# Optimization experiments

Hardware: AMD Instinct MI355X
Metric: run time of the kernel (lower is better)

Reference implementation:

```python
import jax, jax.numpy as jnp
import numpy as np

K = 3          # kernel size
SIZE = K * K   # 9 taps
STEPS = 10     # max_step
EPS = 1e-5


def _unfold3x3(x):
    # x: [n, c, h, w] -> patches [n, c, 9, h, w], same order as F.unfold (row-major taps)
    n, c, h, w = x.shape
    xp = jnp.pad(x, ((0, 0), (0, 0), (1, 1), (1, 1)))
    return jnp.stack([xp[:, :, di:di + h, dj:dj + w]
                      for di in range(K) for dj in range(K)], axis=2)


def setup_inputs() -> dict:
    key = jax.random.key(0)
    k1, k2 = jax.random.split(key)
    n, c, h, w = 8, 64, 128, 128
    inp = jax.random.normal(k1, (n, c, h, w), dtype=jnp.float32)
    weight = jax.random.uniform(k2, (n, SIZE, h, w), dtype=jnp.float32)  # wc=1
    return {"input": inp, "weight": weight}


def reference(input, weight):
    n, c, h, w = input.shape
    wc = weight.shape[1] // SIZE  # = 1
    wt = weight.reshape(n, wc, SIZE, h, w)
    # normalize taps to sum to 1 per pixel (non-sym_norm branch)
    norm_weight = wt / (jnp.sum(wt, axis=2, keepdims=True) + EPS)  # [n,1,9,h,w]
    x = input
    for _ in range(STEPS):
        patches = _unfold3x3(x)                 # [n,c,9,h,w]
        x = jnp.sum(patches * norm_weight, axis=2)  # [n,c,h,w]
    return x
```

## Files before the change

### kernel.cpp

```cpp
#include <hip/hip_runtime.h>
#include <hip/hip_fp16.h>


#define NB    8
#define CC    64
#define HH    128
#define WW    128
#define TAPS  9
#define PLANE (HH * WW)

#define CORE   16
#define HALO5  5
#define RROWS  26
#define RSTR4  129
#define NTH    832
#define NSTEP  5
#define CGRP   16
#define CSUB   8
#define WROWS  24
#define WCELLS (WROWS * TAPS * 32)

#define PERM4(J) ((((J) & 3) << 5) | ((J) >> 2))

typedef unsigned int u32x4 __attribute__((ext_vector_type(4)));

#define MIXLO(acc, xh, wf)                                                      \
    asm("v_fma_mix_f32 %0, %1, %2, %0 op_sel:[0,0,0] op_sel_hi:[1,0,0]"         \
        : "+v"(acc) : "v"(xh), "v"(wf))
#define MIXHI(acc, xh, wf)                                                      \
    asm("v_fma_mix_f32 %0, %1, %2, %0 op_sel:[1,0,0] op_sel_hi:[1,0,0]"         \
        : "+v"(acc) : "v"(xh), "v"(wf))
#define MIX8(aL, aH, cell, wf)                                                  \
    MIXLO(aL.x, cell.x, wf); MIXHI(aL.y, cell.x, wf);                           \
    MIXLO(aL.z, cell.y, wf); MIXHI(aL.w, cell.y, wf);                           \
    MIXLO(aH.x, cell.z, wf); MIXHI(aH.y, cell.z, wf);                           \
    MIXLO(aH.z, cell.w, wf); MIXHI(aH.w, cell.w, wf)

__device__ __forceinline__ float4 cvt_lo(const uint4 v) {
    const float2 a = __half22float2(*reinterpret_cast<const __half2*>(&v.x));
    const float2 b = __half22float2(*reinterpret_cast<const __half2*>(&v.y));
    return make_float4(a.x, a.y, b.x, b.y);
}
__device__ __forceinline__ float4 cvt_hi(const uint4 v) {
    const float2 a = __half22float2(*reinterpret_cast<const __half2*>(&v.z));
    const float2 b = __half22float2(*reinterpret_cast<const __half2*>(&v.w));
    return make_float4(a.x, a.y, b.x, b.y);
}
__device__ __forceinline__ unsigned pack2(float a, float b) {
    __half2 h = __floats2half2_rn(a, b);
    return *reinterpret_cast<unsigned*>(&h);
}
__device__ __forceinline__ float2 h22f2(unsigned u) {
    return __half22float2(*reinterpret_cast<const __half2*>(&u));
}

__global__ __launch_bounds__(256) void mp_norm_kernel(const float* __restrict__ w,
                                                      uint2* __restrict__ nwh) {
    int tid = blockIdx.x * 256 + threadIdx.x;
    int wg = tid & 31;
    int h  = (tid >> 5) & 127;
    int n  = tid >> 12;
    int base = n * TAPS * PLANE + h * WW + wg * 4;
    float4 t[TAPS];
    float sx = 1e-5f, sy = 1e-5f, sz = 1e-5f, sw = 1e-5f;
#pragma unroll
    for (int k = 0; k < TAPS; ++k) {
        t[k] = *reinterpret_cast<const float4*>(w + base + k * PLANE);
        sx += t[k].x; sy += t[k].y; sz += t[k].z; sw += t[k].w;
    }
    float rx = 1.0f / sx, ry = 1.0f / sy, rz = 1.0f / sz, rw = 1.0f / sw;
#pragma unroll
    for (int k = 0; k < TAPS; ++k) {
        uint2 v;
        v.x = pack2(t[k].x * rx, t[k].y * ry);
        v.y = pack2(t[k].z * rz, t[k].w * rw);
        nwh[((n * TAPS + k) * HH + h) * 32 + wg] = v;
    }
}

#define FUSED_PROLOGUE                                                          \
    __shared__ uint4 bufA[RROWS * RSTR4];                                       \
    __shared__ uint4 bufB[RROWS * RSTR4];                                       \
    __shared__ uint2 wlds[WCELLS];                                              \
    const int bid = blockIdx.x;                                                 \
    const int n   = bid & 7;                                                    \
    const int ht  = (bid >> 3) & 7;                                             \
    const int cg  = bid >> 6;                                                   \
    const int tr0 = ht * CORE;                                                  \
    const int cb  = cg * CGRP;                                                  \
    const int t   = threadIdx.x;                                                \
    const int row = t >> 5;                                                     \
    const int s   = t & 31;                                                     \
    {                                                                           \
        const uint2* nwb = nwh + (size_t)n * TAPS * (PLANE / 4);                \
        for (int idx = t; idx < WCELLS; idx += NTH) {                           \
            const int wrow = idx / (TAPS * 32);                                 \
            const int rem  = idx - wrow * (TAPS * 32);                          \
            const int k    = rem >> 5;                                          \
            const int ss   = rem & 31;                                          \
            const int gr   = tr0 - (HALO5 - 1) + wrow;                          \
            uint2 v = make_uint2(0u, 0u);                                       \
            if (gr >= 0 && gr < HH)                                             \
                v = nwb[(k * HH + gr) * 32 + ss];                               \
            wlds[idx] = v;                                                      \
        }                                                                       \
    }                                                                           \
    const uint4 zc = make_uint4(0u, 0u, 0u, 0u);                                \
    const float4 z = make_float4(0.f, 0.f, 0.f, 0.f);

#define FUSED_STEPS                                                             \
        uint4* pin  = bufA;                                                     \
        uint4* pout = bufB;                                                     \
        for (int st = 0; st < NSTEP; ++st) {                                    \
            const int lo = st + 1;                                              \
            const int hi = 24 - st;                                             \
            if (row >= lo && row <= hi) {                                       \
                int wb = (row - 1) * (TAPS * 32) + s;                           \
                asm volatile("" : "+v"(wb));                                    \
                float4 aL0 = z, aL1 = z, aL2 = z, aL3 = z;                      \
                float4 aH0 = z, aH1 = z, aH2 = z, aH3 = z;                      \
                _Pragma("unroll")                                               \
                for (int di = 0; di < 3; ++di) {                                \
                    const uint4* rp = pin + (row - 1 + di) * RSTR4;             \
                    uint4 x[6];                                                 \
                    x[0] = (s > 0) ? rp[96 + s - 1] : zc;                       \
                    x[1] = rp[s];                                               \
                    x[2] = rp[32 + s];                                          \
                    x[3] = rp[64 + s];                                          \
                    x[4] = rp[96 + s];                                          \
                    x[5] = (s < 31) ? rp[s + 1] : zc;                           \
                    _Pragma("unroll")                                           \
                    for (int dj = 0; dj < 3; ++dj) {                            \
                        const int k = di * 3 + dj;                              \
                        const uint2 wv = wlds[wb + k * 32];                     \
                        const float2 w01 = h22f2(wv.x);                         \
                        const float2 w23 = h22f2(wv.y);                         \
                        MIX8(aL0, aH0, x[0 + dj], w01.x);                       \
                        MIX8(aL1, aH1, x[1 + dj], w01.y);                       \
                        MIX8(aL2, aH2, x[2 + dj], w23.x);                       \
                        MIX8(aL3, aH3, x[3 + dj], w23.y);                       \
                    }                                                           \
                }                                                               \
                uint4* op = pout + row * RSTR4;                                 \
                uint4 o0, o1, o2, o3;                                           \
                o0.x = pack2(aL0.x, aL0.y); o0.y = pack2(aL0.z, aL0.w);         \
                o0.z = pack2(aH0.x, aH0.y); o0.w = pack2(aH0.z, aH0.w);         \
                o1.x = pack2(aL1.x, aL1.y); o1.y = pack2(aL1.z, aL1.w);         \
                o1.z = pack2(aH1.x, aH1.y); o1.w = pack2(aH1.z, aH1.w);         \
                o2.x = pack2(aL2.x, aL2.y); o2.y = pack2(aL2.z, aL2.w);         \
                o2.z = pack2(aH2.x, aH2.y); o2.w = pack2(aH2.z, aH2.w);         \
                o3.x = pack2(aL3.x, aL3.y); o3.y = pack2(aL3.z, aL3.w);         \
                o3.z = pack2(aH3.x, aH3.y); o3.w = pack2(aH3.z, aH3.w);         \
                op[s]      = o0;                                                \
                op[32 + s] = o1;                                                \
                op[64 + s] = o2;                                                \
                op[96 + s] = o3;                                                \
            }                                                                   \
            __syncthreads();                                                    \
            uint4* tmp = pin; pin = pout; pout = tmp;                           \
        }

__global__ __launch_bounds__(NTH, 1) void mp_fused5_a(const float* __restrict__ src,
                                                      uint4* __restrict__ dst16,
                                                      const uint2* __restrict__ nwh) {
    FUSED_PROLOGUE
    for (int ch = 0; ch < CGRP; ch += CSUB) {
        const float* sp = src + ((size_t)n * CC + cb + ch) * PLANE;
        for (int idx = t; idx < RROWS * WW; idx += NTH) {
            const int r  = idx >> 7;
            const int J  = idx & 127;
            const int gr = tr0 - HALO5 + r;
            uint4 v = zc;
            if (gr >= 0 && gr < HH) {
                const int o = gr * WW + J;
                v.x = pack2(sp[o],             sp[PLANE + o]);
                v.y = pack2(sp[2 * PLANE + o], sp[3 * PLANE + o]);
                v.z = pack2(sp[4 * PLANE + o], sp[5 * PLANE + o]);
                v.w = pack2(sp[6 * PLANE + o], sp[7 * PLANE + o]);
            }
            bufA[r * RSTR4 + PERM4(J)] = v;
        }
        __syncthreads();
        FUSED_STEPS
        uint4* dp16 = dst16 + ((size_t)n * (CC / 8) + ((cb + ch) >> 3)) * PLANE;
        for (int idx = t; idx < CORE * WW; idx += NTH) {
            const int r = idx >> 7;
            const int J = idx & 127;
            dp16[(tr0 + r) * WW + J] = pin[(r + HALO5) * RSTR4 + PERM4(J)];
        }
        __syncthreads();
    }
}

__global__ __launch_bounds__(NTH, 1) void mp_fused5_b(const uint4* __restrict__ src16,
                                                      float* __restrict__ dst,
                                                      const uint2* __restrict__ nwh) {
    FUSED_PROLOGUE
#pragma unroll 1
    for (int ch = 0; ch < CGRP; ch += CSUB) {
        const volatile u32x4* sp16v =
            (const volatile u32x4*)(src16 + ((size_t)n * (CC / 8) + ((cb + ch) >> 3)) * PLANE);
        for (int idx = t; idx < RROWS * WW; idx += NTH) {
            const int r  = idx >> 7;
            const int J  = idx & 127;
            const int gr = tr0 - HALO5 + r;
            uint4 v = zc;
            if (gr >= 0 && gr < HH) {
                const u32x4 w = sp16v[gr * WW + J];
                v = make_uint4(w.x, w.y, w.z, w.w);
            }
            bufA[r * RSTR4 + PERM4(J)] = v;
        }
        __syncthreads();
        FUSED_STEPS
        float* dp = dst + ((size_t)n * CC + cb + ch) * PLANE;
        for (int idx = t; idx < CORE * WW; idx += NTH) {
            const int r = idx >> 7;
            const int J = idx & 127;
            const uint4 v = pin[(r + HALO5) * RSTR4 + PERM4(J)];
            const float4 lo = cvt_lo(v);
            const float4 hi = cvt_hi(v);
            const int o = (tr0 + r) * WW + J;
            dp[o]             = lo.x;
            dp[PLANE + o]     = lo.y;
            dp[2 * PLANE + o] = lo.z;
            dp[3 * PLANE + o] = lo.w;
            dp[4 * PLANE + o] = hi.x;
            dp[5 * PLANE + o] = hi.y;
            dp[6 * PLANE + o] = hi.z;
            dp[7 * PLANE + o] = hi.w;
        }
        __syncthreads();
    }
}

extern "C" void kernel_launch(void* const* d_in, const int* in_sizes, int n_in,
                              void* d_out, int out_size, void* d_ws, size_t ws_size,
                              hipStream_t stream) {
    const float* input  = (const float*)d_in[0];
    const float* weight = (const float*)d_in[1];
    float* out = (float*)d_out;

    uint2* nwh = (uint2*)d_ws;
    uint4* B0  = (uint4*)((char*)d_ws + (size_t)NB * TAPS * PLANE * 2);

    mp_norm_kernel<<<128, 256, 0, stream>>>(weight, nwh);
    mp_fused5_a<<<256, NTH, 0, stream>>>(input, B0, nwh);
    mp_fused5_b<<<256, NTH, 0, stream>>>(B0, out, nwh);
}
```

Measured before the change: 87.72 us.

## Split 8-channel fp16 LDS cells into two 4-channel planes processed sequentially

Replaces each uint4 shared-memory cell holding eight fp16 channels with two separate uint2 planes of four channels each. The stencil body now runs twice per step, once per plane, keeping four accumulator float4s live instead of eight. The intermediate global buffer between the two fused kernels becomes two 4-channel planes as well. The aim is to reduce register pressure and LDS access width, at the cost of loading the weights and neighbour indices twice per step and issuing more, narrower LDS and global accesses.

```diff
diff --git a/kernel.cpp b/kernel.cpp
--- a/kernel.cpp
+++ b/kernel.cpp
@@ -22,7 +22,7 @@
 
 #define PERM4(J) ((((J) & 3) << 5) | ((J) >> 2))
 
-typedef unsigned int u32x4 __attribute__((ext_vector_type(4)));
+typedef unsigned int u32x2 __attribute__((ext_vector_type(2)));
 
 #define MIXLO(acc, xh, wf)                                                      \
     asm("v_fma_mix_f32 %0, %1, %2, %0 op_sel:[0,0,0] op_sel_hi:[1,0,0]"         \
@@ -30,22 +30,10 @@
 #define MIXHI(acc, xh, wf)                                                      \
     asm("v_fma_mix_f32 %0, %1, %2, %0 op_sel:[1,0,0] op_sel_hi:[1,0,0]"         \
         : "+v"(acc) : "v"(xh), "v"(wf))
-#define MIX8(aL, aH, cell, wf)                                                  \
-    MIXLO(aL.x, cell.x, wf); MIXHI(aL.y, cell.x, wf);                           \
-    MIXLO(aL.z, cell.y, wf); MIXHI(aL.w, cell.y, wf);                           \
-    MIXLO(aH.x, cell.z, wf); MIXHI(aH.y, cell.z, wf);                           \
-    MIXLO(aH.z, cell.w, wf); MIXHI(aH.w, cell.w, wf)
-
-__device__ __forceinline__ float4 cvt_lo(const uint4 v) {
-    const float2 a = __half22float2(*reinterpret_cast<const __half2*>(&v.x));
-    const float2 b = __half22float2(*reinterpret_cast<const __half2*>(&v.y));
-    return make_float4(a.x, a.y, b.x, b.y);
-}
-__device__ __forceinline__ float4 cvt_hi(const uint4 v) {
-    const float2 a = __half22float2(*reinterpret_cast<const __half2*>(&v.z));
-    const float2 b = __half22float2(*reinterpret_cast<const __half2*>(&v.w));
-    return make_float4(a.x, a.y, b.x, b.y);
-}
+#define MIX4(a, cell, wf)                                                       \
+    MIXLO(a.x, cell.x, wf); MIXHI(a.y, cell.x, wf);                             \
+    MIXLO(a.z, cell.y, wf); MIXHI(a.w, cell.y, wf)
+
 __device__ __forceinline__ unsigned pack2(float a, float b) {
     __half2 h = __floats2half2_rn(a, b);
     return *reinterpret_cast<unsigned*>(&h);
@@ -79,9 +67,11 @@
 }
 
 #define FUSED_PROLOGUE                                                          \
-    __shared__ uint4 bufA[RROWS * RSTR4];                                       \
-    __shared__ uint4 bufB[RROWS * RSTR4];                                       \
-    __shared__ uint2 wlds[WCELLS];                                              \
+    __shared__ uint2 xA0[RROWS * RSTR4];                     \
+    __shared__ uint2 xB0[RROWS * RSTR4];                                        \
+    __shared__ uint2 xA1[RROWS * RSTR4];                                        \
+    __shared__ uint2 xB1[RROWS * RSTR4];                                        \
+    __shared__ uint2 wlds[WCELLS];             \
     const int bid = blockIdx.x;                                                 \
     const int n   = bid & 7;                                                    \
     const int ht  = (bid >> 3) & 7;                                             \
@@ -105,63 +95,58 @@
             wlds[idx] = v;                                                      \
         }                                                                       \
     }                                                                           \
-    const uint4 zc = make_uint4(0u, 0u, 0u, 0u);                                \
-    const float4 z = make_float4(0.f, 0.f, 0.f, 0.f);
+    const uint2 zc2 = make_uint2(0u, 0u);                                       \
+    const float4 z  = make_float4(0.f, 0.f, 0.f, 0.f);
+
+#define SUB_BODY(PIN, POUT)                                                     \
+            {                                                                   \
+                float4 a0 = z, a1 = z, a2 = z, a3 = z;                          \
+                _Pragma("unroll")                                               \
+                for (int di = 0; di < 3; ++di) {                                \
+                    const uint2* rp = PIN + (row - 1 + di) * RSTR4;             \
+                    uint2 x[6];                                                 \
+                    x[0] = (s > 0) ? rp[96 + s - 1] : zc2;                      \
+                    x[1] = rp[s];                                               \
+                    x[2] = rp[32 + s];                                          \
+                    x[3] = rp[64 + s];                                          \
+                    x[4] = rp[96 + s];                                          \
+                    x[5] = (s < 31) ? rp[s + 1] : zc2;                          \
+                    _Pragma("unroll")                                           \
+                    for (int dj = 0; dj < 3; ++dj) {                            \
+                        const uint2 wv = wlds[wb + (di * 3 + dj) * 32];         \
+                        const float2 w01 = h22f2(wv.x);                         \
+                        const float2 w23 = h22f2(wv.y);                         \
+                        MIX4(a0, x[0 + dj], w01.x);                             \
+                        MIX4(a1, x[1 + dj], w01.y);                             \
+                        MIX4(a2, x[2 + dj], w23.x);                             \
+                        MIX4(a3, x[3 + dj], w23.y);                             \
+                    }                                                           \
+                }                                                               \
+                uint2* op = POUT + row * RSTR4;                                 \
+                op[s]      = make_uint2(pack2(a0.x, a0.y), pack2(a0.z, a0.w));  \
+                op[32 + s] = make_uint2(pack2(a1.x, a1.y), pack2(a1.z, a1.w));  \
+                op[64 + s] = make_uint2(pack2(a2.x, a2.y), pack2(a2.z, a2.w));  \
+                op[96 + s] = make_uint2(pack2(a3.x, a3.y), pack2(a3.z, a3.w));  \
+            }
 
 #define FUSED_STEPS                                                             \
-        uint4* pin  = bufA;                                                     \
-        uint4* pout = bufB;                                                     \
+        uint2 *pin0 = xA0, *pout0 = xB0, *pin1 = xA1, *pout1 = xB1;             \
         for (int st = 0; st < NSTEP; ++st) {                                    \
             const int lo = st + 1;                                              \
             const int hi = 24 - st;                                             \
             if (row >= lo && row <= hi) {                                       \
                 int wb = (row - 1) * (TAPS * 32) + s;                           \
                 asm volatile("" : "+v"(wb));                                    \
-                float4 aL0 = z, aL1 = z, aL2 = z, aL3 = z;                      \
-                float4 aH0 = z, aH1 = z, aH2 = z, aH3 = z;                      \
-                _Pragma("unroll")                                               \
-                for (int di = 0; di < 3; ++di) {                                \
-                    const uint4* rp = pin + (row - 1 + di) * RSTR4;             \
-                    uint4 x[6];                                                 \
-                    x[0] = (s > 0) ? rp[96 + s - 1] : zc;                       \
-                    x[1] = rp[s];                                               \
-                    x[2] = rp[32 + s];                                          \
-                    x[3] = rp[64 + s];                                          \
-                    x[4] = rp[96 + s];                                          \
-                    x[5] = (s < 31) ? rp[s + 1] : zc;                           \
-                    _Pragma("unroll")                                           \
-                    for (int dj = 0; dj < 3; ++dj) {                            \
-                        const int k = di * 3 + dj;                              \
-                        const uint2 wv = wlds[wb + k * 32];                     \
-                        const float2 w01 = h22f2(wv.x);                         \
-                        const float2 w23 = h22f2(wv.y);                         \
-                        MIX8(aL0, aH0, x[0 + dj], w01.x);                       \
-                        MIX8(aL1, aH1, x[1 + dj], w01.y);                       \
-                        MIX8(aL2, aH2, x[2 + dj], w23.x);                       \
-                        MIX8(aL3, aH3, x[3 + dj], w23.y);                       \
-                    }                                                           \
-                }                                                               \
-                uint4* op = pout + row * RSTR4;                                 \
-                uint4 o0, o1, o2, o3;                                           \
-                o0.x = pack2(aL0.x, aL0.y); o0.y = pack2(aL0.z, aL0.w);         \
-                o0.z = pack2(aH0.x, aH0.y); o0.w = pack2(aH0.z, aH0.w);         \
-                o1.x = pack2(aL1.x, aL1.y); o1.y = pack2(aL1.z, aL1.w);         \
-                o1.z = pack2(aH1.x, aH1.y); o1.w = pack2(aH1.z, aH1.w);         \
-                o2.x = pack2(aL2.x, aL2.y); o2.y = pack2(aL2.z, aL2.w);         \
-                o2.z = pack2(aH2.x, aH2.y); o2.w = pack2(aH2.z, aH2.w);         \
-                o3.x = pack2(aL3.x, aL3.y); o3.y = pack2(aL3.z, aL3.w);         \
-                o3.z = pack2(aH3.x, aH3.y); o3.w = pack2(aH3.z, aH3.w);         \
-                op[s]      = o0;                                                \
-                op[32 + s] = o1;                                                \
-                op[64 + s] = o2;                                                \
-                op[96 + s] = o3;                                                \
+                SUB_BODY(pin0, pout0)                                           \
+                SUB_BODY(pin1, pout1)                                           \
             }                                                                   \
             __syncthreads();                                                    \
-            uint4* tmp = pin; pin = pout; pout = tmp;                           \
+            uint2* t0 = pin0; pin0 = pout0; pout0 = t0;                         \
+            uint2* t1 = pin1; pin1 = pout1; pout1 = t1;                         \
         }
 
 __global__ __launch_bounds__(NTH, 1) void mp_fused5_a(const float* __restrict__ src,
-                                                      uint4* __restrict__ dst16,
+                                                      uint2* __restrict__ dst16,
                                                       const uint2* __restrict__ nwh) {
     FUSED_PROLOGUE
     for (int ch = 0; ch < CGRP; ch += CSUB) {
@@ -170,46 +155,59 @@
             const int r  = idx >> 7;
             const int J  = idx & 127;
             const int gr = tr0 - HALO5 + r;
-            uint4 v = zc;
+            uint2 v0 = zc2, v1 = zc2;
             if (gr >= 0 && gr < HH) {
                 const int o = gr * WW + J;
-                v.x = pack2(sp[o],             sp[PLANE + o]);
-                v.y = pack2(sp[2 * PLANE + o], sp[3 * PLANE + o]);
-                v.z = pack2(sp[4 * PLANE + o], sp[5 * PLANE + o]);
-                v.w = pack2(sp[6 * PLANE + o], sp[7 * PLANE + o]);
+                v0.x = pack2(sp[o],             sp[PLANE + o]);
+                v0.y = pack2(sp[2 * PLANE + o], sp[3 * PLANE + o]);
+                v1.x = pack2(sp[4 * PLANE + o], sp[5 * PLANE + o]);
+                v1.y = pack2(sp[6 * PLANE + o], sp[7 * PLANE + o]);
             }
-            bufA[r * RSTR4 + PERM4(J)] = v;
+            const int c = r * RSTR4 + PERM4(J);
+            xA0[c] = v0;
+            xA1[c] = v1;
         }
         __syncthreads();
         FUSED_STEPS
-        uint4* dp16 = dst16 + ((size_t)n * (CC / 8) + ((cb + ch) >> 3)) * PLANE;
+        const int q = (cb + ch) >> 2;
+        uint2* dp0 = dst16 + ((size_t)n * (CC / 4) + q) * PLANE;
+        uint2* dp1 = dp0 + PLANE;
         for (int idx = t; idx < CORE * WW; idx += NTH) {
             const int r = idx >> 7;
             const int J = idx & 127;
-            dp16[(tr0 + r) * WW + J] = pin[(r + HALO5) * RSTR4 + PERM4(J)];
-        }
-        __syncthreads();
-    }
-}
-
-__global__ __launch_bounds__(NTH, 1) void mp_fused5_b(const uint4* __restrict__ src16,
+            const int c = (r + HALO5) * RSTR4 + PERM4(J);
+            const int o = (tr0 + r) * WW + J;
+            dp0[o] = pin0[c];
+            dp1[o] = pin1[c];
+        }
+        __syncthreads();
+    }
+}
+
+__global__ __launch_bounds__(NTH, 1) void mp_fused5_b(const uint2* __restrict__ src16,
                                                       float* __restrict__ dst,
                                                       const uint2* __restrict__ nwh) {
     FUSED_PROLOGUE
 #pragma unroll 1
     for (int ch = 0; ch < CGRP; ch += CSUB) {
-        const volatile u32x4* sp16v =
-            (const volatile u32x4*)(src16 + ((size_t)n * (CC / 8) + ((cb + ch) >> 3)) * PLANE);
+        const int q = (cb + ch) >> 2;
+        const volatile u32x2* s0 =
+            (const volatile u32x2*)(src16 + ((size_t)n * (CC / 4) + q) * PLANE);
+        const volatile u32x2* s1 = s0 + PLANE;
         for (int idx = t; idx < RROWS * WW; idx += NTH) {
             const int r  = idx >> 7;
             const int J  = idx & 127;
             const int gr = tr0 - HALO5 + r;
-            uint4 v = zc;
+            uint2 v0 = zc2, v1 = zc2;
             if (gr >= 0 && gr < HH) {
-                const u32x4 w = sp16v[gr * WW + J];
-                v = make_uint4(w.x, w.y, w.z, w.w);
+                const u32x2 w0 = s0[gr * WW + J];
+                const u32x2 w1 = s1[gr * WW + J];
+                v0 = make_uint2(w0.x, w0.y);
+                v1 = make_uint2(w1.x, w1.y);
             }
-            bufA[r * RSTR4 + PERM4(J)] = v;
+            const int c = r * RSTR4 + PERM4(J);
+            xA0[c] = v0;
+            xA1[c] = v1;
         }
         __syncthreads();
         FUSED_STEPS
@@ -217,18 +215,22 @@
         for (int idx = t; idx < CORE * WW; idx += NTH) {
             const int r = idx >> 7;
             const int J = idx & 127;
-            const uint4 v = pin[(r + HALO5) * RSTR4 + PERM4(J)];
-            const float4 lo = cvt_lo(v);
-            const float4 hi = cvt_hi(v);
+            const int c = (r + HALO5) * RSTR4 + PERM4(J);
+            const uint2 v0 = pin0[c];
+            const uint2 v1 = pin1[c];
+            const float2 c01 = h22f2(v0.x);
+            const float2 c23 = h22f2(v0.y);
+            const float2 c45 = h22f2(v1.x);
+            const float2 c67 = h22f2(v1.y);
             const int o = (tr0 + r) * WW + J;
-            dp[o]             = lo.x;
-            dp[PLANE + o]     = lo.y;
-            dp[2 * PLANE + o] = lo.z;
-            dp[3 * PLANE + o] = lo.w;
-            dp[4 * PLANE + o] = hi.x;
-            dp[5 * PLANE + o] = hi.y;
-            dp[6 * PLANE + o] = hi.z;
-            dp[7 * PLANE + o] = hi.w;
+            dp[o]             = c01.x;
+            dp[PLANE + o]     = c01.y;
+            dp[2 * PLANE + o] = c23.x;
+            dp[3 * PLANE + o] = c23.y;
+            dp[4 * PLANE + o] = c45.x;
+            dp[5 * PLANE + o] = c45.y;
+            dp[6 * PLANE + o] = c67.x;
+            dp[7 * PLANE + o] = c67.y;
         }
         __syncthreads();
     }
@@ -242,7 +244,7 @@
     float* out = (float*)d_out;
 
     uint2* nwh = (uint2*)d_ws;
-    uint4* B0  = (uint4*)((char*)d_ws + (size_t)NB * TAPS * PLANE * 2);
+    uint2* B0  = (uint2*)((char*)d_ws + (size_t)NB * TAPS * PLANE * 2);
 
     mp_norm_kernel<<<128, 256, 0, stream>>>(weight, nwh);
     mp_fused5_a<<<256, NTH, 0, stream>>>(input, B0, nwh);
```

After: 93.26 us. 1.06x slower.
